# Kernel tuning notes

Hardware: AMD Instinct MI355X
Metric: run time of the kernel (lower is better)

The kernel has to match this reference:

```python
import jax, jax.numpy as jnp
import numpy as np

H = W = 2048        # voxel grid
P0 = 0.1            # occupancy density
EPS = 1e-5          # BatchNorm eps (torch default)


def _grid(rs, cs):
    g = np.full((H, W), -1, np.int64)
    g[rs, cs] = np.arange(rs.size)
    return g


def _conv_map(g, rs, cs, s):
    # kernel map for 3x3 conv at tensor stride s: offsets {-s,0,s}^2, -1 = missing neighbor
    maps = []
    for dr in (-s, 0, s):
        for dc in (-s, 0, s):
            r2, c2 = rs + dr, cs + dc
            ok = (r2 >= 0) & (r2 < H) & (c2 >= 0) & (c2 < W)
            m = np.full(rs.size, -1, np.int64)
            m[ok] = g[r2[ok], c2[ok]]
            maps.append(m)
    return np.stack(maps, 1)  # [N, 9]


def _pool_map(g, rs, cs, s):
    # 2x2 max pool stride 2 at tensor stride s: out coords = floor to multiples of 2s
    out = np.unique(np.stack([rs - rs % (2 * s), cs - cs % (2 * s)], 1), axis=0)
    maps = []
    for dr in (0, s):
        for dc in (0, s):
            r2, c2 = out[:, 0] + dr, out[:, 1] + dc
            ok = (r2 < H) & (c2 < W)
            m = np.full(out.shape[0], -1, np.int64)
            m[ok] = g[r2[ok], c2[ok]]
            maps.append(m)
    return out, np.stack(maps, 1)  # coords, [N_out, 4]


def _build_maps():
    rng = np.random.default_rng(0)
    n0 = int(H * W * P0)
    flat = rng.choice(H * W, size=n0, replace=False)
    flat.sort()
    rs0, cs0 = np.divmod(flat, W)
    g0 = _grid(rs0, cs0)
    nbr0 = _conv_map(g0, rs0, cs0, 1)
    c1, pmap1 = _pool_map(g0, rs0, cs0, 1)
    g1 = _grid(c1[:, 0], c1[:, 1])
    nbr1 = _conv_map(g1, c1[:, 0], c1[:, 1], 2)
    c2, pmap2 = _pool_map(g1, c1[:, 0], c1[:, 1], 2)
    return n0, nbr0, pmap1, nbr1, pmap2, c2.shape[0]


def setup_inputs() -> dict:
    n0, nbr0, pmap1, nbr1, pmap2, n2 = _build_maps()
    key = jax.random.key(0)
    k0, k1, k2, k3 = jax.random.split(key, 4)
    f0 = jax.random.normal(k0, (n0, 1), jnp.float32)
    W1 = jax.random.normal(k1, (9, 1, 8), jnp.float32) * 0.3
    W2 = jax.random.normal(k2, (9, 8, 16), jnp.float32) * 0.12
    Wfc = jax.random.normal(k3, (16, 2), jnp.float32) * 0.25
    return dict(
        f0=f0, W1=W1, b1=jnp.zeros((8,), jnp.float32),
        gamma1=jnp.ones((8,), jnp.float32), beta1=jnp.zeros((8,), jnp.float32),
        W2=W2, b2=jnp.zeros((16,), jnp.float32),
        gamma2=jnp.ones((16,), jnp.float32), beta2=jnp.zeros((16,), jnp.float32),
        Wfc=Wfc, bfc=jnp.zeros((2,), jnp.float32),
        nbr0=jnp.asarray(nbr0), pmap1=jnp.asarray(pmap1),
        nbr1=jnp.asarray(nbr1), pmap2=jnp.asarray(pmap2),
    )


def _sparse_conv(f, nbr, Wk, b):
    # gather-matmul-scatter: missing neighbors contribute zero
    n = f.shape[0]
    fpad = jnp.concatenate([f, jnp.zeros((1, f.shape[1]), f.dtype)], 0)
    g = fpad[jnp.where(nbr < 0, n, nbr)]  # [N_out, 9, C_in]
    return jnp.einsum('nkc,kcd->nd', g, Wk) + b


def _bn_relu(x, gamma, beta):
    mu = x.mean(0)
    var = x.var(0)  # biased, as torch BN normalization
    return jax.nn.relu((x - mu) * jax.lax.rsqrt(var + EPS) * gamma + beta)


def _max_pool(f, pmap):
    # max over existing children only (every output has >= 1 child)
    n = f.shape[0]
    fpad = jnp.concatenate([f, jnp.full((1, f.shape[1]), -jnp.inf, f.dtype)], 0)
    return fpad[jnp.where(pmap < 0, n, pmap)].max(1)


def reference(f0, W1, b1, gamma1, beta1, W2, b2, gamma2, beta2, Wfc, bfc,
              nbr0, pmap1, nbr1, pmap2):
    x = _bn_relu(_sparse_conv(f0, nbr0, W1, b1), gamma1, beta1)
    x = _max_pool(x, pmap1)
    x = _bn_relu(_sparse_conv(x, nbr1, W2, b2), gamma2, beta2)
    x = _max_pool(x, pmap2)
    return x @ Wfc + bfc
```

## Files before the change

kernel.cpp:

```cpp
#include <hip/hip_runtime.h>

#define EPS 1e-5f
#define NSLOT 64
#define FLT_BIG 3.402823466e+38f

__device__ __forceinline__ float waveReduceSum(float v) {
    #pragma unroll
    for (int off = 32; off > 0; off >>= 1)
        v += __shfl_down(v, off, 64);
    return v;
}

template <int NV>
__device__ __forceinline__ float statReduce(float (&v)[NV], int lane) {
    #pragma unroll
    for (int b = 0; (1 << b) < NV; ++b) {
        const int d = 1 << b;
        const bool hi = (lane >> b) & 1;
        #pragma unroll
        for (int i = 0; i < (NV >> (b + 1)); ++i) {
            float kept = hi ? v[2 * i + 1] : v[2 * i];
            float sent = hi ? v[2 * i] : v[2 * i + 1];
            float recv = __shfl_xor(sent, d, 64);
            v[i] = kept + recv;
        }
    }
    float r = v[0];
    #pragma unroll
    for (int d = NV; d < 64; d <<= 1)
        r += __shfl_xor(r, d, 64);
    return r;
}

__global__ __launch_bounds__(256) void k_zero(float4* __restrict__ slots) {
    const float4 z4 = {0.f, 0.f, 0.f, 0.f};
    #pragma unroll
    for (int q = 0; q < 4; ++q)
        slots[q * 256 + threadIdx.x] = z4;
}

__global__ __launch_bounds__(256, 4) void k_conv1pool(
        const float* __restrict__ f0, const float* __restrict__ W1,
        const float* __restrict__ b1, const float* __restrict__ gamma1,
        const int* __restrict__ nbr0, const int* __restrict__ pmap1,
        float* __restrict__ pmm, float* __restrict__ slots, int n1) {
    __shared__ float sred[16];
    int t = threadIdx.x;
    int lane = t & 63;
    if (t < 16) sred[t] = 0.f;
    __syncthreads();

    int i = blockIdx.x * blockDim.x + t;
    bool valid = (i < n1);
    int icl = valid ? i : (n1 - 1);
    int4 pm = ((const int4*)pmap1)[icl];
    if (!valid) { pm.x = -1; pm.y = -1; pm.z = -1; pm.w = -1; }
    int ch[4] = {pm.x, pm.y, pm.z, pm.w};

    float maxv[8], minv[8], red[16];
    #pragma unroll
    for (int c = 0; c < 8; ++c) { maxv[c] = -FLT_BIG; minv[c] = FLT_BIG; }
    #pragma unroll
    for (int c = 0; c < 16; ++c) red[c] = 0.f;

    #pragma unroll
    for (int p = 0; p < 2; ++p) {
        int c0 = ch[2 * p], c1 = ch[2 * p + 1];
        int j0 = c0 >= 0 ? c0 : 0;
        int j1 = c1 >= 0 ? c1 : 0;
        int idx0[9], idx1[9];
        #pragma unroll
        for (int k = 0; k < 9; ++k) idx0[k] = nbr0[(size_t)j0 * 9 + k];
        #pragma unroll
        for (int k = 0; k < 9; ++k) idx1[k] = nbr0[(size_t)j1 * 9 + k];
        float v0[9], v1[9];
        #pragma unroll
        for (int k = 0; k < 9; ++k) {
            int e = idx0[k]; float f = f0[e >= 0 ? e : 0]; v0[k] = e >= 0 ? f : 0.f;
        }
        #pragma unroll
        for (int k = 0; k < 9; ++k) {
            int e = idx1[k]; float f = f0[e >= 0 ? e : 0]; v1[k] = e >= 0 ? f : 0.f;
        }
        float a0[8], a1[8];
        #pragma unroll
        for (int c = 0; c < 8; ++c) { a0[c] = b1[c]; a1[c] = b1[c]; }
        #pragma unroll
        for (int k = 0; k < 9; ++k) {
            #pragma unroll
            for (int c = 0; c < 8; ++c) {
                float w = W1[k * 8 + c];
                a0[c] = fmaf(v0[k], w, a0[c]);
                a1[c] = fmaf(v1[k], w, a1[c]);
            }
        }
        if (c0 >= 0) {
            #pragma unroll
            for (int c = 0; c < 8; ++c) {
                red[c] += a0[c]; red[8 + c] += a0[c] * a0[c];
                maxv[c] = fmaxf(maxv[c], a0[c]); minv[c] = fminf(minv[c], a0[c]);
            }
        }
        if (c1 >= 0) {
            #pragma unroll
            for (int c = 0; c < 8; ++c) {
                red[c] += a1[c]; red[8 + c] += a1[c] * a1[c];
                maxv[c] = fmaxf(maxv[c], a1[c]); minv[c] = fminf(minv[c], a1[c]);
            }
        }
    }

    if (valid) {
        float sel[8];
        #pragma unroll
        for (int c = 0; c < 8; ++c)
            sel[c] = (gamma1[c] >= 0.f) ? maxv[c] : minv[c];
        float4* dst = (float4*)(pmm + (size_t)i * 8);
        dst[0] = make_float4(sel[0], sel[1], sel[2], sel[3]);
        dst[1] = make_float4(sel[4], sel[5], sel[6], sel[7]);
    }

    float tot = statReduce<16>(red, lane);
    if (lane < 16) atomicAdd(&sred[lane], tot);
    __syncthreads();
    if (t < 16)
        atomicAdd(&slots[(size_t)(blockIdx.x & (NSLOT - 1)) * 64 + t], sred[t]);
}

__global__ __launch_bounds__(256, 4) void k_conv2(
        const float* __restrict__ pmm, const float* __restrict__ W2,
        const float* __restrict__ b2, const int* __restrict__ nbr1,
        const float* __restrict__ gamma1, const float* __restrict__ beta1,
        float* __restrict__ x2, float* __restrict__ slots, int n1, float invn0) {
    __shared__ float sred[32];
    __shared__ float sstat[16];
    int t = threadIdx.x;
    int lane = t & 63;
    if (t < 32) sred[t] = 0.f;
    if (t < 64) {
        const float4* s4 = (const float4*)(slots + (size_t)t * 64);
        float4 a = s4[0], b = s4[1], c4 = s4[2], d = s4[3];
        float vals[16] = {a.x, a.y, a.z, a.w, b.x, b.y, b.z, b.w,
                          c4.x, c4.y, c4.z, c4.w, d.x, d.y, d.z, d.w};
        #pragma unroll
        for (int c = 0; c < 16; ++c) {
            float s = waveReduceSum(vals[c]);
            if (t == 0) sstat[c] = s;
        }
    }
    __syncthreads();

    float bm[8], sc[8], bb[8];
    #pragma unroll
    for (int c = 0; c < 8; ++c) {
        float mu  = sstat[c] * invn0;
        float var = sstat[8 + c] * invn0 - mu * mu;
        bm[c] = mu;
        sc[c] = rsqrtf(var + EPS) * gamma1[c];
        bb[c] = beta1[c];
    }

    int n = blockIdx.x * blockDim.x + t;
    bool valid = (n < n1);
    int nn = valid ? n : (n1 - 1);

    int idx[9];
    #pragma unroll
    for (int k = 0; k < 9; ++k) idx[k] = nbr1[(size_t)nn * 9 + k];

    float acc[16];
    #pragma unroll
    for (int c = 0; c < 16; ++c) acc[c] = b2[c];

    #pragma unroll
    for (int k = 0; k < 9; ++k) {
        const float4* base =
            (const float4*)(pmm + (size_t)(idx[k] >= 0 ? idx[k] : 0) * 8);
        float4 P0 = base[0], P1 = base[1];
        float pv[8] = {P0.x, P0.y, P0.z, P0.w, P1.x, P1.y, P1.z, P1.w};
        float g[8];
        #pragma unroll
        for (int c = 0; c < 8; ++c) {
            float z = fmaxf(fmaf(pv[c] - bm[c], sc[c], bb[c]), 0.f);
            g[c] = (idx[k] >= 0) ? z : 0.f;
        }
        #pragma unroll
        for (int ci = 0; ci < 8; ++ci) {
            #pragma unroll
            for (int c = 0; c < 16; ++c)
                acc[c] = fmaf(g[ci], W2[(k * 8 + ci) * 16 + c], acc[c]);
        }
    }

    if (valid) {
        float4* dst = (float4*)(x2 + (size_t)n * 16);
        #pragma unroll
        for (int q4 = 0; q4 < 4; ++q4) {
            float4 v = {acc[q4 * 4], acc[q4 * 4 + 1],
                        acc[q4 * 4 + 2], acc[q4 * 4 + 3]};
            dst[q4] = v;
        }
    } else {
        #pragma unroll
        for (int c = 0; c < 16; ++c) acc[c] = 0.f;
    }

    float red[32];
    #pragma unroll
    for (int c = 0; c < 16; ++c) {
        red[c] = acc[c];
        red[16 + c] = acc[c] * acc[c];
    }
    float tot = statReduce<32>(red, lane);
    if (lane < 32) atomicAdd(&sred[lane], tot);
    __syncthreads();
    if (t < 32)
        atomicAdd(&slots[(size_t)(blockIdx.x & (NSLOT - 1)) * 64 + 16 + t], sred[t]);
}

__global__ __launch_bounds__(256) void k_pool2_fc(
        const float* __restrict__ x2, const int* __restrict__ pmap2,
        const float* __restrict__ slots, const float* __restrict__ gamma2,
        const float* __restrict__ beta2, const float* __restrict__ Wfc,
        const float* __restrict__ bfc, float* __restrict__ out,
        int n2, float invn) {
    __shared__ float sstat[32];
    int t = threadIdx.x;
    if (t < 64) {
        const float4* s4 = (const float4*)(slots + (size_t)t * 64 + 16);
        float vals[32];
        #pragma unroll
        for (int q = 0; q < 8; ++q) {
            float4 a = s4[q];
            vals[q * 4 + 0] = a.x; vals[q * 4 + 1] = a.y;
            vals[q * 4 + 2] = a.z; vals[q * 4 + 3] = a.w;
        }
        #pragma unroll
        for (int c = 0; c < 32; ++c) {
            float s = waveReduceSum(vals[c]);
            if (t == 0) sstat[c] = s;
        }
    }
    __syncthreads();

    int i = blockIdx.x * blockDim.x + t;
    if (i >= n2) return;

    float m[16], sc[16], bb[16];
    #pragma unroll
    for (int c = 0; c < 16; ++c) {
        float mu  = sstat[c] * invn;
        float var = sstat[16 + c] * invn - mu * mu;
        m[c]  = mu;
        sc[c] = rsqrtf(var + EPS) * gamma2[c];
        bb[c] = beta2[c];
    }

    int4 pm = ((const int4*)pmap2)[i];
    int idx[4] = {pm.x, pm.y, pm.z, pm.w};
    float best[16];
    #pragma unroll
    for (int c = 0; c < 16; ++c) best[c] = 0.f;
    #pragma unroll
    for (int k = 0; k < 4; ++k) {
        int j = idx[k] >= 0 ? idx[k] : 0;
        const float4* src = (const float4*)(x2 + (size_t)j * 16);
        #pragma unroll
        for (int q4 = 0; q4 < 4; ++q4) {
            float4 v4 = src[q4];
            float v[4] = {v4.x, v4.y, v4.z, v4.w};
            #pragma unroll
            for (int c = 0; c < 4; ++c) {
                int cc = q4 * 4 + c;
                float z = fmaxf(fmaf(v[c] - m[cc], sc[cc], bb[cc]), 0.f);
                z = (idx[k] >= 0) ? z : 0.f;
                best[cc] = fmaxf(best[cc], z);
            }
        }
    }
    float o0 = bfc[0], o1 = bfc[1];
    #pragma unroll
    for (int c = 0; c < 16; ++c) {
        o0 = fmaf(best[c], Wfc[c * 2 + 0], o0);
        o1 = fmaf(best[c], Wfc[c * 2 + 1], o1);
    }
    out[(size_t)i * 2 + 0] = o0;
    out[(size_t)i * 2 + 1] = o1;
}

extern "C" void kernel_launch(void* const* d_in, const int* in_sizes, int n_in,
                              void* d_out, int out_size, void* d_ws, size_t ws_size,
                              hipStream_t stream) {
    const float* f0     = (const float*)d_in[0];
    const float* W1     = (const float*)d_in[1];
    const float* b1     = (const float*)d_in[2];
    const float* gamma1 = (const float*)d_in[3];
    const float* beta1  = (const float*)d_in[4];
    const float* W2     = (const float*)d_in[5];
    const float* b2     = (const float*)d_in[6];
    const float* gamma2 = (const float*)d_in[7];
    const float* beta2  = (const float*)d_in[8];
    const float* Wfc    = (const float*)d_in[9];
    const float* bfc    = (const float*)d_in[10];
    const int*   nbr0   = (const int*)d_in[11];
    const int*   pmap1  = (const int*)d_in[12];
    const int*   nbr1   = (const int*)d_in[13];
    const int*   pmap2  = (const int*)d_in[14];

    const int n0 = in_sizes[0];
    const int n1 = in_sizes[12] / 4;
    const int n2 = in_sizes[14] / 4;

    float* ws    = (float*)d_ws;
    float* slots = ws;
    float* pmm   = ws + (size_t)NSLOT * 64;
    float* x2    = pmm + (size_t)n1 * 8;

    const int B = 256;
    k_zero<<<1, B, 0, stream>>>((float4*)slots);
    k_conv1pool<<<(n1 + B - 1) / B, B, 0, stream>>>(f0, W1, b1, gamma1, nbr0, pmap1,
                                                    pmm, slots, n1);
    k_conv2<<<(n1 + B - 1) / B, B, 0, stream>>>(pmm, W2, b2, nbr1, gamma1, beta1,
                                                x2, slots, n1, 1.0f / (float)n0);
    k_pool2_fc<<<(n2 + B - 1) / B, B, 0, stream>>>(x2, pmap2, slots, gamma2, beta2,
                                                   Wfc, bfc, (float*)d_out,
                                                   n2, 1.0f / (float)n1);
}
```

Before: 78.06 us.

## Precompute BN1 scale/shift in tiny kernel; process two points per thread in conv2

Moves the BN1 statistics reduction out of every conv2 block into a single small kernel that writes a folded scale and shift per channel. conv2 then handles two output points per thread, so each W2 weight load feeds two accumulators and there is more memory-level parallelism per thread. The cost is an extra kernel launch, higher register pressure under launch_bounds(256,4), and half as many blocks.

```diff
diff --git a/kernel.cpp b/kernel.cpp
--- a/kernel.cpp
+++ b/kernel.cpp
@@ -127,89 +127,108 @@
         atomicAdd(&slots[(size_t)(blockIdx.x & (NSLOT - 1)) * 64 + t], sred[t]);
 }
 
+__global__ __launch_bounds__(64) void k_bn1stats(
+        const float* __restrict__ slots, const float* __restrict__ gamma1,
+        const float* __restrict__ beta1, float* __restrict__ stats, float invn0) {
+    __shared__ float st[16];
+    int t = threadIdx.x;
+    if (t < 16) {
+        float s = 0.f;
+        #pragma unroll 8
+        for (int k = 0; k < NSLOT; ++k) s += slots[(size_t)k * 64 + t];
+        st[t] = s;
+    }
+    __syncthreads();
+    if (t < 8) {
+        float mu  = st[t] * invn0;
+        float var = st[8 + t] * invn0 - mu * mu;
+        float sc  = rsqrtf(var + EPS) * gamma1[t];
+        stats[t]     = sc;
+        stats[8 + t] = beta1[t] - sc * mu;
+    }
+}
+
 __global__ __launch_bounds__(256, 4) void k_conv2(
         const float* __restrict__ pmm, const float* __restrict__ W2,
         const float* __restrict__ b2, const int* __restrict__ nbr1,
-        const float* __restrict__ gamma1, const float* __restrict__ beta1,
-        float* __restrict__ x2, float* __restrict__ slots, int n1, float invn0) {
+        const float* __restrict__ stats, float* __restrict__ x2,
+        float* __restrict__ slots, int n1) {
     __shared__ float sred[32];
-    __shared__ float sstat[16];
     int t = threadIdx.x;
     int lane = t & 63;
     if (t < 32) sred[t] = 0.f;
-    if (t < 64) {
-        const float4* s4 = (const float4*)(slots + (size_t)t * 64);
-        float4 a = s4[0], b = s4[1], c4 = s4[2], d = s4[3];
-        float vals[16] = {a.x, a.y, a.z, a.w, b.x, b.y, b.z, b.w,
-                          c4.x, c4.y, c4.z, c4.w, d.x, d.y, d.z, d.w};
-        #pragma unroll
-        for (int c = 0; c < 16; ++c) {
-            float s = waveReduceSum(vals[c]);
-            if (t == 0) sstat[c] = s;
-        }
-    }
-    __syncthreads();
-
-    float bm[8], sc[8], bb[8];
-    #pragma unroll
-    for (int c = 0; c < 8; ++c) {
-        float mu  = sstat[c] * invn0;
-        float var = sstat[8 + c] * invn0 - mu * mu;
-        bm[c] = mu;
-        sc[c] = rsqrtf(var + EPS) * gamma1[c];
-        bb[c] = beta1[c];
-    }
-
-    int n = blockIdx.x * blockDim.x + t;
-    bool valid = (n < n1);
-    int nn = valid ? n : (n1 - 1);
-
-    int idx[9];
-    #pragma unroll
-    for (int k = 0; k < 9; ++k) idx[k] = nbr1[(size_t)nn * 9 + k];
-
-    float acc[16];
-    #pragma unroll
-    for (int c = 0; c < 16; ++c) acc[c] = b2[c];
+    __syncthreads();
+
+    int nA = blockIdx.x * 512 + t;
+    int nB = nA + 256;
+    bool vA = (nA < n1), vB = (nB < n1);
+    int iA = vA ? nA : (n1 - 1);
+    int iB = vB ? nB : (n1 - 1);
+
+    int idxA[9], idxB[9];
+    #pragma unroll
+    for (int k = 0; k < 9; ++k) idxA[k] = nbr1[(size_t)iA * 9 + k];
+    #pragma unroll
+    for (int k = 0; k < 9; ++k) idxB[k] = nbr1[(size_t)iB * 9 + k];
+
+    float accA[16], accB[16];
+    #pragma unroll
+    for (int c = 0; c < 16; ++c) { accA[c] = b2[c]; accB[c] = b2[c]; }
 
     #pragma unroll
     for (int k = 0; k < 9; ++k) {
-        const float4* base =
-            (const float4*)(pmm + (size_t)(idx[k] >= 0 ? idx[k] : 0) * 8);
-        float4 P0 = base[0], P1 = base[1];
-        float pv[8] = {P0.x, P0.y, P0.z, P0.w, P1.x, P1.y, P1.z, P1.w};
-        float g[8];
+        const float4* bA = (const float4*)(pmm + (size_t)(idxA[k] >= 0 ? idxA[k] : 0) * 8);
+        const float4* bB = (const float4*)(pmm + (size_t)(idxB[k] >= 0 ? idxB[k] : 0) * 8);
+        float4 A0 = bA[0], A1 = bA[1];
+        float4 B0 = bB[0], B1 = bB[1];
+        float pA[8] = {A0.x, A0.y, A0.z, A0.w, A1.x, A1.y, A1.z, A1.w};
+        float pB[8] = {B0.x, B0.y, B0.z, B0.w, B1.x, B1.y, B1.z, B1.w};
+        float gA[8], gB[8];
         #pragma unroll
         for (int c = 0; c < 8; ++c) {
-            float z = fmaxf(fmaf(pv[c] - bm[c], sc[c], bb[c]), 0.f);
-            g[c] = (idx[k] >= 0) ? z : 0.f;
+            float scc = stats[c], b0c = stats[8 + c];
+            float zA = fmaxf(fmaf(pA[c], scc, b0c), 0.f);
+            float zB = fmaxf(fmaf(pB[c], scc, b0c), 0.f);
+            gA[c] = (idxA[k] >= 0) ? zA : 0.f;
+            gB[c] = (idxB[k] >= 0) ? zB : 0.f;
         }
         #pragma unroll
         for (int ci = 0; ci < 8; ++ci) {
             #pragma unroll
-            for (int c = 0; c < 16; ++c)
-                acc[c] = fmaf(g[ci], W2[(k * 8 + ci) * 16 + c], acc[c]);
-        }
-    }
-
-    if (valid) {
-        float4* dst = (float4*)(x2 + (size_t)n * 16);
-        #pragma unroll
-        for (int q4 = 0; q4 < 4; ++q4) {
-            float4 v = {acc[q4 * 4], acc[q4 * 4 + 1],
-                        acc[q4 * 4 + 2], acc[q4 * 4 + 3]};
-            dst[q4] = v;
-        }
+            for (int c = 0; c < 16; ++c) {
+                float w = W2[(k * 8 + ci) * 16 + c];
+                accA[c] = fmaf(gA[ci], w, accA[c]);
+                accB[c] = fmaf(gB[ci], w, accB[c]);
+            }
+        }
+    }
+
+    if (vA) {
+        float4* dst = (float4*)(x2 + (size_t)nA * 16);
+        #pragma unroll
+        for (int q4 = 0; q4 < 4; ++q4)
+            dst[q4] = make_float4(accA[q4 * 4], accA[q4 * 4 + 1],
+                                  accA[q4 * 4 + 2], accA[q4 * 4 + 3]);
     } else {
         #pragma unroll
-        for (int c = 0; c < 16; ++c) acc[c] = 0.f;
+        for (int c = 0; c < 16; ++c) accA[c] = 0.f;
+    }
+    if (vB) {
+        float4* dst = (float4*)(x2 + (size_t)nB * 16);
+        #pragma unroll
+        for (int q4 = 0; q4 < 4; ++q4)
+            dst[q4] = make_float4(accB[q4 * 4], accB[q4 * 4 + 1],
+                                  accB[q4 * 4 + 2], accB[q4 * 4 + 3]);
+    } else {
+        #pragma unroll
+        for (int c = 0; c < 16; ++c) accB[c] = 0.f;
     }
 
     float red[32];
     #pragma unroll
     for (int c = 0; c < 16; ++c) {
-        red[c] = acc[c];
-        red[16 + c] = acc[c] * acc[c];
+        red[c] = accA[c] + accB[c];
+        red[16 + c] = accA[c] * accA[c] + accB[c] * accB[c];
     }
     float tot = statReduce<32>(red, lane);
     if (lane < 32) atomicAdd(&sred[lane], tot);
@@ -313,15 +332,17 @@
 
     float* ws    = (float*)d_ws;
     float* slots = ws;
-    float* pmm   = ws + (size_t)NSLOT * 64;
+    float* stats = ws + (size_t)NSLOT * 64;
+    float* pmm   = stats + 16;
     float* x2    = pmm + (size_t)n1 * 8;
 
     const int B = 256;
     k_zero<<<1, B, 0, stream>>>((float4*)slots);
     k_conv1pool<<<(n1 + B - 1) / B, B, 0, stream>>>(f0, W1, b1, gamma1, nbr0, pmap1,
                                                     pmm, slots, n1);
-    k_conv2<<<(n1 + B - 1) / B, B, 0, stream>>>(pmm, W2, b2, nbr1, gamma1, beta1,
-                                                x2, slots, n1, 1.0f / (float)n0);
+    k_bn1stats<<<1, 64, 0, stream>>>(slots, gamma1, beta1, stats, 1.0f / (float)n0);
+    k_conv2<<<(n1 + 511) / 512, B, 0, stream>>>(pmm, W2, b2, nbr1, stats,
+                                                x2, slots, n1);
     k_pool2_fc<<<(n2 + B - 1) / B, B, 0, stream>>>(x2, pmap2, slots, gamma2, beta2,
                                                    Wfc, bfc, (float*)d_out,
                                                    n2, 1.0f / (float)n1);
```

After: 256.4 us. 228% more time.
